# Optimization experiments

Measured on AMD Instinct MI355X. Metric: run time of the kernel, lower is better.

## Reference

```python
import jax, jax.numpy as jnp
import numpy as np

WS = 7      # window size
SHIFT = 3   # shift size
H = 56
W = 56
NH = 16     # num heads


def _layernorm(x, g, b):
    m = x.mean(-1, keepdims=True)
    v = x.var(-1, keepdims=True)
    return (x - m) / jnp.sqrt(v + 1e-5) * g + b


def setup_inputs() -> dict:
    key = jax.random.key(0)
    ks = jax.random.split(key, 8)
    B, C = 16, 512
    DH = 4 * C
    s = 0.02
    x = jax.random.normal(ks[0], (B, H * W, C), jnp.float32)

    # relative position index (matches torch buffer construction)
    coords = np.stack(np.meshgrid(np.arange(WS), np.arange(WS), indexing='ij')).reshape(2, -1)
    rel = (coords[:, :, None] - coords[:, None, :]).transpose(1, 2, 0).copy()
    rel[..., 0] += WS - 1
    rel[..., 1] += WS - 1
    rel[..., 0] *= 2 * WS - 1
    rpi = jnp.asarray(rel.sum(-1), jnp.int32)  # (49, 49)

    # shifted-window additive attention mask (nW, N, N)
    img = np.zeros((H, W))
    cnt = 0
    for hs in (slice(0, -WS), slice(-WS, -SHIFT), slice(-SHIFT, None)):
        for wsl in (slice(0, -WS), slice(-WS, -SHIFT), slice(-SHIFT, None)):
            img[hs, wsl] = cnt
            cnt += 1
    mw = img.reshape(H // WS, WS, W // WS, WS).transpose(0, 2, 1, 3).reshape(-1, WS * WS)
    diff = mw[:, None, :] - mw[:, :, None]  # == mw.unsqueeze(1) - mw.unsqueeze(2)
    attn_mask = jnp.asarray(np.where(diff != 0, -100.0, 0.0), jnp.float32)

    return {
        'x': x,
        'rpi': rpi,
        'attn_mask': attn_mask,
        'norm1_g': jnp.ones((C,), jnp.float32),
        'norm1_b': jnp.zeros((C,), jnp.float32),
        'qkv_w': jax.random.normal(ks[1], (3 * C, C), jnp.float32) * s,
        'qkv_b': jnp.zeros((3 * C,), jnp.float32),
        'proj_w': jax.random.normal(ks[2], (C, C), jnp.float32) * s,
        'proj_b': jnp.zeros((C,), jnp.float32),
        'rpb_table': jax.random.normal(ks[3], ((2 * WS - 1) ** 2, NH), jnp.float32) * s,
        'norm2_g': jnp.ones((C,), jnp.float32),
        'norm2_b': jnp.zeros((C,), jnp.float32),
        'mlp_w1': jax.random.normal(ks[4], (DH, C), jnp.float32) * s,
        'mlp_b1': jnp.zeros((DH,), jnp.float32),
        'mlp_w2': jax.random.normal(ks[5], (C, DH), jnp.float32) * s,
        'mlp_b2': jnp.zeros((C,), jnp.float32),
    }


def reference(x, rpi, attn_mask, norm1_g, norm1_b, qkv_w, qkv_b, proj_w, proj_b,
              rpb_table, norm2_g, norm2_b, mlp_w1, mlp_b1, mlp_w2, mlp_b2):
    B, L, C = x.shape
    N = WS * WS
    nW = (H // WS) * (W // WS)
    hd = C // NH

    # --- attention branch ---
    h = _layernorm(x, norm1_g, norm1_b).reshape(B, H, W, C)
    h = jnp.roll(h, (-SHIFT, -SHIFT), axis=(1, 2))
    # window partition -> (B*nW, N, C)
    xw = h.reshape(B, H // WS, WS, W // WS, WS, C).transpose(0, 1, 3, 2, 4, 5).reshape(B * nW, N, C)

    qkv = (xw @ qkv_w.T + qkv_b).reshape(B * nW, N, 3, NH, hd).transpose(2, 0, 3, 1, 4)
    q, k, v = qkv[0], qkv[1], qkv[2]  # (B*nW, NH, N, hd)
    attn = jnp.einsum('bhnd,bhmd->bhnm', q * (hd ** -0.5), k)
    rpb = rpb_table[rpi].transpose(2, 0, 1)  # (NH, N, N)
    attn = attn + rpb[None]
    attn = attn.reshape(B, nW, NH, N, N) + attn_mask[None, :, None]
    attn = jax.nn.softmax(attn.reshape(B * nW, NH, N, N), axis=-1)
    o = jnp.einsum('bhnm,bhmd->bhnd', attn, v).transpose(0, 2, 1, 3).reshape(B * nW, N, C)
    o = o @ proj_w.T + proj_b
    # window reverse + unshift
    o = o.reshape(B, H // WS, W // WS, WS, WS, C).transpose(0, 1, 3, 2, 4, 5).reshape(B, H, W, C)
    o = jnp.roll(o, (SHIFT, SHIFT), axis=(1, 2)).reshape(B, L, C)

    x = x + o
    # --- MLP branch ---
    h2 = _layernorm(x, norm2_g, norm2_b)
    m = jax.nn.gelu(h2 @ mlp_w1.T + mlp_b1, approximate=False)
    return x + (m @ mlp_w2.T + mlp_b2)
```

## Files before the change

kernel.cpp:

```cpp
#include <hip/hip_runtime.h>
#include <hip/hip_bf16.h>

typedef __attribute__((ext_vector_type(8))) short bf16x8_t;
typedef __attribute__((ext_vector_type(4))) float f32x4_t;

#define LD8(p) (*(const bf16x8_t*)(p))

__device__ __forceinline__ void gll16(const void* g, void* l) {
  __builtin_amdgcn_global_load_lds((const __attribute__((address_space(1))) void*)g,
                                   (__attribute__((address_space(3))) void*)l, 16, 0, 0);
}

__global__ __launch_bounds__(256) void k_cvt(const float* __restrict__ in,
                                             __hip_bfloat16* __restrict__ out, int n) {
  int i = blockIdx.x * 256 + threadIdx.x;
  if (i < n) out[i] = __float2bfloat16(in[i]);
}

__global__ __launch_bounds__(256) void k_cmb(const int* __restrict__ rpi,
                                             const float* __restrict__ tab,
                                             const float* __restrict__ mask,
                                             float* __restrict__ cmbp) {
  int idx = blockIdx.x * 256 + threadIdx.x;
  int jj = idx & 3, lane = (idx >> 2) & 63, tile = (idx >> 8) & 15;
  int h = (idx >> 12) & 15, w6 = idx >> 16;
  int r = (tile >> 2) * 16 + (lane >> 4) * 4 + jj;
  int c = (tile & 3) * 16 + (lane & 15);
  float v = -1e9f;
  if (r < 49 && c < 49) v = tab[rpi[r * 49 + c] * 16 + h] + mask[w6 * 2401 + r * 49 + c];
  cmbp[idx] = v;
}

template<int PERM>
__global__ __launch_bounds__(256) void k_ln(const float* __restrict__ in,
                                            const float* __restrict__ g,
                                            const float* __restrict__ bta,
                                            __hip_bfloat16* __restrict__ out) {
  int token = blockIdx.x;
  int t = threadIdx.x;
  const float2 v = ((const float2*)(in + (size_t)token * 512))[t];
  float s = v.x + v.y, sq = v.x * v.x + v.y * v.y;
  #pragma unroll
  for (int d = 1; d < 64; d <<= 1) { s += __shfl_xor(s, d); sq += __shfl_xor(sq, d); }
  __shared__ float ps[4], pq[4];
  int w = t >> 6;
  if ((t & 63) == 0) { ps[w] = s; pq[w] = sq; }
  __syncthreads();
  s  = ps[0] + ps[1] + ps[2] + ps[3];
  sq = pq[0] + pq[1] + pq[2] + pq[3];
  float mean = s * (1.f / 512.f);
  float inv = rsqrtf(sq * (1.f / 512.f) - mean * mean + 1e-5f);
  size_t dst;
  if (PERM) {
    int b = token / 3136, p = token - b * 3136;
    int i = p / 56, j = p - i * 56;
    int gi = (i + 53) % 56, gj = (j + 53) % 56;
    dst = ((size_t)(((b * 64) + (gi / 7) * 8 + (gj / 7)) * 49) + (gi % 7) * 7 + (gj % 7)) * 512;
  } else {
    dst = (size_t)token * 512;
  }
  int c = t * 2;
  out[dst + c]     = __float2bfloat16((v.x - mean) * inv * g[c] + bta[c]);
  out[dst + c + 1] = __float2bfloat16((v.y - mean) * inv * g[c + 1] + bta[c + 1]);
}

__global__ __launch_bounds__(256) void k_attn(const __hip_bfloat16* __restrict__ qkv,
                                              const float* __restrict__ cmbp,
                                              __hip_bfloat16* __restrict__ o) {
  __shared__ __align__(16) __hip_bfloat16 vt_all[4 * 32 * 72];
  __shared__ __align__(16) __hip_bfloat16 P_all[4 * 64 * 72];
  const int t = threadIdx.x, l = t & 63, w = t >> 6;
  const int bw = blockIdx.x;
  const int head = blockIdx.y * 4 + w;
  const int rr = l & 15, g = l >> 4;
  __hip_bfloat16* vt = vt_all + w * (32 * 72);
  __hip_bfloat16* P  = P_all  + w * (64 * 72);
  const __hip_bfloat16* base = qkv + (size_t)bw * 49 * 1536 + head * 32;
  const bf16x8_t zero8 = {};

  { int d = l >> 1, sg = (l & 1) * 8;
    *(bf16x8_t*)(vt + d * 72 + 48 + sg) = zero8; }
  __builtin_amdgcn_sched_barrier(0);
  #pragma unroll
  for (int it = 0; it < 4; ++it) {
    int idx = l + it * 64;
    if (idx < 196) {
      int j = idx >> 2, sg = (idx & 3) * 8;
      bf16x8_t vv = *(const bf16x8_t*)(base + 1024 + (size_t)j * 1536 + sg);
      #pragma unroll
      for (int s2 = 0; s2 < 8; ++s2) vt[(sg + s2) * 72 + j] = ((__hip_bfloat16*)&vv)[s2];
    }
  }
  bf16x8_t aq[4], bk[4];
  #pragma unroll
  for (int m = 0; m < 4; ++m) {
    int row = m * 16 + rr;
    aq[m] = (row < 49) ? *(const bf16x8_t*)(base + (size_t)row * 1536 + g * 8) : zero8;
    bk[m] = (row < 49) ? *(const bf16x8_t*)(base + 512 + (size_t)row * 1536 + g * 8) : zero8;
  }
  const float4* cp = (const float4*)(cmbp + (size_t)((bw & 63) * 16 + head) * 4096);
  f32x4_t S[4][4];
  #pragma unroll
  for (int tm = 0; tm < 4; ++tm)
    #pragma unroll
    for (int tn = 0; tn < 4; ++tn) {
      float4 cv = cp[(tm * 4 + tn) * 64 + l];
      f32x4_t c0 = { cv.x, cv.y, cv.z, cv.w };
      S[tm][tn] = __builtin_amdgcn_mfma_f32_16x16x32_bf16(aq[tm], bk[tn], c0, 0, 0, 0);
    }
  float sm[4][4];
  #pragma unroll
  for (int tm = 0; tm < 4; ++tm) {
    #pragma unroll
    for (int jj = 0; jj < 4; ++jj) {
      float v = fmaxf(fmaxf(S[tm][0][jj], S[tm][1][jj]), fmaxf(S[tm][2][jj], S[tm][3][jj]));
      v = fmaxf(v, __shfl_xor(v, 1));
      v = fmaxf(v, __shfl_xor(v, 2));
      v = fmaxf(v, __shfl_xor(v, 4));
      v = fmaxf(v, __shfl_xor(v, 8));
      float s = 0.f;
      #pragma unroll
      for (int tn = 0; tn < 4; ++tn) {
        float e = __expf(S[tm][tn][jj] - v);
        S[tm][tn][jj] = e;
        s += e;
      }
      s += __shfl_xor(s, 1); s += __shfl_xor(s, 2); s += __shfl_xor(s, 4); s += __shfl_xor(s, 8);
      sm[tm][jj] = s;
    }
  }
  #pragma unroll
  for (int tm = 0; tm < 4; ++tm)
    #pragma unroll
    for (int tn = 0; tn < 4; ++tn)
      #pragma unroll
      for (int jj = 0; jj < 4; ++jj)
        P[(tm * 16 + g * 4 + jj) * 72 + tn * 16 + rr] = __float2bfloat16(S[tm][tn][jj]);

  f32x4_t O[4][2] = {};
  #pragma unroll
  for (int ks = 0; ks < 2; ++ks) {
    bf16x8_t pa[4], vb[2];
    #pragma unroll
    for (int tm = 0; tm < 4; ++tm)
      pa[tm] = *(const bf16x8_t*)(P + (tm * 16 + rr) * 72 + ks * 32 + g * 8);
    #pragma unroll
    for (int tn = 0; tn < 2; ++tn)
      vb[tn] = *(const bf16x8_t*)(vt + (tn * 16 + rr) * 72 + ks * 32 + g * 8);
    #pragma unroll
    for (int tm = 0; tm < 4; ++tm)
      #pragma unroll
      for (int tn = 0; tn < 2; ++tn)
        O[tm][tn] = __builtin_amdgcn_mfma_f32_16x16x32_bf16(pa[tm], vb[tn], O[tm][tn], 0, 0, 0);
  }
  #pragma unroll
  for (int tm = 0; tm < 4; ++tm) {
    #pragma unroll
    for (int jj = 0; jj < 4; ++jj) {
      int r = tm * 16 + g * 4 + jj;
      if (r < 49) {
        float rcp = 1.f / sm[tm][jj];
        size_t ob = ((size_t)bw * 49 + r) * 512 + head * 32;
        o[ob + rr]      = __float2bfloat16(O[tm][0][jj] * rcp);
        o[ob + 16 + rr] = __float2bfloat16(O[tm][1][jj] * rcp);
      }
    }
  }
}

template<int EP>
__global__ __launch_bounds__(512, 2) void gemm256(const __hip_bfloat16* __restrict__ A,
                                                  const __hip_bfloat16* __restrict__ Bw,
                                                  int K, int Ncols, int nNB,
                                                  const float* __restrict__ bias,
                                                  __hip_bfloat16* __restrict__ obf,
                                                  const float* __restrict__ resid,
                                                  float* __restrict__ ofp) {
  __shared__ __align__(16) char LDS[131072];
  const int nwg = gridDim.x, orig = blockIdx.x;
  const int q8 = nwg >> 3, r8 = nwg & 7;
  const int xcd = orig & 7, lin = orig >> 3;
  const int wgid = (xcd < r8 ? xcd * (q8 + 1) : r8 * (q8 + 1) + (xcd - r8) * q8) + lin;
  const int bx = wgid / nNB, by = wgid - bx * nNB;
  const int m0 = bx * 256, n0 = by * 256;
  const int t = threadIdx.x, l = t & 63, w = t >> 6;
  const int wr = w >> 2, wc = w & 3;
  const int rr = l & 15, kq = l >> 4;
  const int swzo = (kq * 16) ^ ((rr & 8) << 2);

  int rs0, cs0, rs1, cs1;
  { int d = t * 16;  rs0 = (d >> 10) * 16 + ((d >> 6) & 15);
    cs0 = ((d & 63) ^ (((d >> 9) & 1) << 5)) >> 1; }
  { int d = 8192 + t * 16; int dd = d & 8191;
    rs1 = (dd >> 10) * 16 + ((dd >> 6) & 15);
    cs1 = 32 + (((d & 63) ^ (((d >> 9) & 1) << 5)) >> 1); }
  const __hip_bfloat16* gA = A + (size_t)m0 * K;
  const __hip_bfloat16* gB = Bw + (size_t)n0 * K;

  auto stageA = [&](int T, int h) {
    char* dst = LDS + (T & 1) * 32768 + h * 16384 + t * 16;
    const size_t kb = (size_t)T * 64;
    gll16(gA + (size_t)(h * 128 + rs0) * K + kb + cs0, dst);
    gll16(gA + (size_t)(h * 128 + rs1) * K + kb + cs1, dst + 8192);
  };
  auto stageB = [&](int T, int h) {
    char* dst = LDS + 65536 + (T & 1) * 32768 + h * 16384 + t * 16;
    const size_t kb = (size_t)T * 64;
    gll16(gB + (size_t)(h * 128 + rs0) * K + kb + cs0, dst);
    gll16(gB + (size_t)(h * 128 + rs1) * K + kb + cs1, dst + 8192);
  };

  auto ldA = [&](bf16x8_t (&a)[4][2], int buf, int mq) {
    const char* b = LDS + buf * 32768 + wr * 16384;
    #pragma unroll
    for (int m = 0; m < 4; ++m)
      #pragma unroll
      for (int ks = 0; ks < 2; ++ks)
        a[m][ks] = *(const bf16x8_t*)(b + ks * 8192 + (mq * 4 + m) * 1024 + rr * 64 + swzo);
  };
  auto ldB = [&](bf16x8_t (&bv)[2][2], int buf, int nq) {
    const char* b = LDS + 65536 + buf * 32768 + (wc >> 1) * 16384;
    #pragma unroll
    for (int n = 0; n < 2; ++n)
      #pragma unroll
      for (int ks = 0; ks < 2; ++ks)
        bv[n][ks] = *(const bf16x8_t*)(b + ks * 8192 + ((wc & 1) * 4 + nq * 2 + n) * 1024 + rr * 64 + swzo);
  };

  f32x4_t acc[8][4] = {};
  auto mma = [&](bf16x8_t (&a)[4][2], bf16x8_t (&bv)[2][2], int mq, int nq) {
    __builtin_amdgcn_s_setprio(1);
    #pragma unroll
    for (int m = 0; m < 4; ++m)
      #pragma unroll
      for (int n = 0; n < 2; ++n)
        #pragma unroll
        for (int ks = 0; ks < 2; ++ks)
          acc[mq * 4 + m][nq * 2 + n] =
            __builtin_amdgcn_mfma_f32_16x16x32_bf16(a[m][ks], bv[n][ks], acc[mq * 4 + m][nq * 2 + n], 0, 0, 0);
    __builtin_amdgcn_s_setprio(0);
  };

  const int NT = K >> 6;
  stageA(0, 0); stageB(0, 0); stageA(0, 1); stageB(0, 1);
  if (1 < NT) { stageA(1, 0); stageB(1, 0); }
  if (1 < NT) asm volatile("s_waitcnt vmcnt(4)" ::: "memory");
  else        asm volatile("s_waitcnt vmcnt(0)" ::: "memory");
  __builtin_amdgcn_s_barrier();

  for (int kt = 0; kt < NT; ++kt) {
    const int cur = kt & 1;
    bf16x8_t Alo[4][2], Ahi[4][2], B0[2][2], B1[2][2];
    ldA(Alo, cur, 0); ldB(B0, cur, 0);
    if (kt + 1 < NT) stageA(kt + 1, 1);
    asm volatile("s_waitcnt lgkmcnt(0)" ::: "memory");
    __builtin_amdgcn_sched_barrier(0);
    mma(Alo, B0, 0, 0);
    ldA(Ahi, cur, 1);
    if (kt + 1 < NT) stageB(kt + 1, 1);
    asm volatile("s_waitcnt lgkmcnt(0)" ::: "memory");
    __builtin_amdgcn_sched_barrier(0);
    mma(Ahi, B0, 1, 0);
    __builtin_amdgcn_s_barrier();
    ldB(B1, cur, 1);
    if (kt + 2 < NT) stageA(kt + 2, 0);
    asm volatile("s_waitcnt lgkmcnt(0)" ::: "memory");
    __builtin_amdgcn_sched_barrier(0);
    mma(Ahi, B1, 1, 1);
    if (kt + 2 < NT) stageB(kt + 2, 0);
    mma(Alo, B1, 0, 1);
    if (kt + 1 < NT) {
      if (kt + 2 < NT) asm volatile("s_waitcnt vmcnt(4)" ::: "memory");
      else             asm volatile("s_waitcnt vmcnt(0)" ::: "memory");
    }
    __builtin_amdgcn_s_barrier();
  }

  #pragma unroll
  for (int m = 0; m < 8; ++m) {
    #pragma unroll
    for (int n = 0; n < 4; ++n) {
      const int gcol = n0 + wc * 64 + n * 16 + rr;
      #pragma unroll
      for (int j = 0; j < 4; ++j) {
        const int grow = m0 + wr * 128 + m * 16 + kq * 4 + j;
        float v = acc[m][n][j] + bias[gcol];
        if (EP == 0) {
          if (gcol < 512) v *= 0.17677669529663687f;
          obf[(size_t)grow * Ncols + gcol] = __float2bfloat16(v);
        } else if (EP == 1) {
          int bw = grow / 49, nn = grow - bw * 49;
          int b = bw >> 6, wi = bw & 63;
          int hh = (wi >> 3) * 7 + nn / 7 + 3;  if (hh >= 56) hh -= 56;
          int ww2 = (wi & 7) * 7 + (nn % 7) + 3; if (ww2 >= 56) ww2 -= 56;
          size_t tok = (size_t)b * 3136 + hh * 56 + ww2;
          ofp[tok * 512 + gcol] = resid[tok * 512 + gcol] + v;
        } else if (EP == 2) {
          float u = 0.5f * v * (1.f + erff(v * 0.70710678118f));
          obf[(size_t)grow * Ncols + gcol] = __float2bfloat16(u);
        } else {
          ofp[(size_t)grow * 512 + gcol] += v;
        }
      }
    }
  }
}

extern "C" void kernel_launch(void* const* d_in, const int* in_sizes, int n_in,
                              void* d_out, int out_size, void* d_ws, size_t ws_size,
                              hipStream_t stream) {
  const float* x      = (const float*)d_in[0];
  const int*   rpi    = (const int*)  d_in[1];
  const float* amask  = (const float*)d_in[2];
  const float* n1g    = (const float*)d_in[3];
  const float* n1b    = (const float*)d_in[4];
  const float* qkv_w  = (const float*)d_in[5];
  const float* qkv_b  = (const float*)d_in[6];
  const float* proj_w = (const float*)d_in[7];
  const float* proj_b = (const float*)d_in[8];
  const float* rpb_t  = (const float*)d_in[9];
  const float* n2g    = (const float*)d_in[10];
  const float* n2b    = (const float*)d_in[11];
  const float* w1     = (const float*)d_in[12];
  const float* b1     = (const float*)d_in[13];
  const float* w2     = (const float*)d_in[14];
  const float* b2     = (const float*)d_in[15];
  float* out = (float*)d_out;

  char* ws = (char*)d_ws;
  const size_t M = 50176;
  const size_t szA = M * 2048 * 2;
  const size_t szB = M * 1536 * 2;
  const size_t offB = szA;
  const size_t offW = offB + szB;
  __hip_bfloat16* bufA = (__hip_bfloat16*)(ws);
  __hip_bfloat16* bufB = (__hip_bfloat16*)(ws + offB);
  __hip_bfloat16* wqkv  = (__hip_bfloat16*)(ws + offW);
  __hip_bfloat16* wproj = wqkv + 786432;
  __hip_bfloat16* wm1   = wproj + 262144;
  __hip_bfloat16* wm2   = wm1 + 1048576;
  float* cmbp = (float*)(ws + szA - (size_t)4194304 * 4);

  k_cvt<<<3072, 256, 0, stream>>>(qkv_w, wqkv, 786432);
  k_cvt<<<1024, 256, 0, stream>>>(proj_w, wproj, 262144);
  k_cvt<<<4096, 256, 0, stream>>>(w1, wm1, 1048576);
  k_cvt<<<4096, 256, 0, stream>>>(w2, wm2, 1048576);
  k_cmb<<<16384, 256, 0, stream>>>(rpi, rpb_t, amask, cmbp);

  k_ln<1><<<50176, 256, 0, stream>>>(x, n1g, n1b, bufA);
  gemm256<0><<<196 * 6, 512, 0, stream>>>(bufA, wqkv, 512, 1536, 6, qkv_b, bufB, nullptr, nullptr);
  k_attn<<<dim3(1024, 4), 256, 0, stream>>>(bufB, cmbp, bufA);
  gemm256<1><<<196 * 2, 512, 0, stream>>>(bufA, wproj, 512, 512, 2, proj_b, nullptr, x, out);
  k_ln<0><<<50176, 256, 0, stream>>>(out, n2g, n2b, bufB);
  gemm256<2><<<196 * 8, 512, 0, stream>>>(bufB, wm1, 512, 2048, 8, b1, bufA, nullptr, nullptr);
  gemm256<3><<<196 * 2, 512, 0, stream>>>(bufA, wm2, 2048, 512, 2, b2, nullptr, nullptr, out);
}
```

Measured before the change: 808.0 us.

## Vectorize layernorm and weight conversion, drop explicit LDS waits in GEMM

New measurement: 761.9 us. 1.06x faster.

```diff
diff --git a/kernel.cpp b/kernel.cpp
--- a/kernel.cpp
+++ b/kernel.cpp
@@ -3,18 +3,29 @@
 
 typedef __attribute__((ext_vector_type(8))) short bf16x8_t;
 typedef __attribute__((ext_vector_type(4))) float f32x4_t;
-
-#define LD8(p) (*(const bf16x8_t*)(p))
 
 __device__ __forceinline__ void gll16(const void* g, void* l) {
   __builtin_amdgcn_global_load_lds((const __attribute__((address_space(1))) void*)g,
                                    (__attribute__((address_space(3))) void*)l, 16, 0, 0);
 }
 
-__global__ __launch_bounds__(256) void k_cvt(const float* __restrict__ in,
-                                             __hip_bfloat16* __restrict__ out, int n) {
-  int i = blockIdx.x * 256 + threadIdx.x;
-  if (i < n) out[i] = __float2bfloat16(in[i]);
+__global__ __launch_bounds__(256) void k_cvt4(const float* __restrict__ s0, const float* __restrict__ s1,
+                                              const float* __restrict__ s2, const float* __restrict__ s3,
+                                              __hip_bfloat16* __restrict__ out) {
+  int i4 = blockIdx.x * 256 + threadIdx.x;
+  int i = i4 * 4;
+  const float* src;
+  int off;
+  if (i < 786432)       { src = s0; off = i; }
+  else if (i < 1048576) { src = s1; off = i - 786432; }
+  else if (i < 2097152) { src = s2; off = i - 1048576; }
+  else                  { src = s3; off = i - 2097152; }
+  float4 v = *(const float4*)(src + off);
+  union { __hip_bfloat16 h[4]; ushort2 u2[2]; } pk;
+  pk.h[0] = __float2bfloat16(v.x); pk.h[1] = __float2bfloat16(v.y);
+  pk.h[2] = __float2bfloat16(v.z); pk.h[3] = __float2bfloat16(v.w);
+  *(ushort2*)(out + i) = pk.u2[0];
+  *(ushort2*)(out + i + 2) = pk.u2[1];
 }
 
 __global__ __launch_bounds__(256) void k_cmb(const int* __restrict__ rpi,
@@ -36,32 +47,38 @@
                                             const float* __restrict__ g,
                                             const float* __restrict__ bta,
                                             __hip_bfloat16* __restrict__ out) {
-  int token = blockIdx.x;
-  int t = threadIdx.x;
-  const float2 v = ((const float2*)(in + (size_t)token * 512))[t];
-  float s = v.x + v.y, sq = v.x * v.x + v.y * v.y;
+  const int w = threadIdx.x >> 6, l = threadIdx.x & 63;
+  const int token = blockIdx.x * 4 + w;
+  const float4* p = (const float4*)(in + (size_t)token * 512);
+  float4 v0 = p[l], v1 = p[l + 64];
+  float s  = v0.x + v0.y + v0.z + v0.w + v1.x + v1.y + v1.z + v1.w;
+  float sq = v0.x*v0.x + v0.y*v0.y + v0.z*v0.z + v0.w*v0.w
+           + v1.x*v1.x + v1.y*v1.y + v1.z*v1.z + v1.w*v1.w;
   #pragma unroll
   for (int d = 1; d < 64; d <<= 1) { s += __shfl_xor(s, d); sq += __shfl_xor(sq, d); }
-  __shared__ float ps[4], pq[4];
-  int w = t >> 6;
-  if ((t & 63) == 0) { ps[w] = s; pq[w] = sq; }
-  __syncthreads();
-  s  = ps[0] + ps[1] + ps[2] + ps[3];
-  sq = pq[0] + pq[1] + pq[2] + pq[3];
   float mean = s * (1.f / 512.f);
   float inv = rsqrtf(sq * (1.f / 512.f) - mean * mean + 1e-5f);
   size_t dst;
   if (PERM) {
-    int b = token / 3136, p = token - b * 3136;
-    int i = p / 56, j = p - i * 56;
+    int b = token / 3136, pp = token - b * 3136;
+    int i = pp / 56, j = pp - i * 56;
     int gi = (i + 53) % 56, gj = (j + 53) % 56;
     dst = ((size_t)(((b * 64) + (gi / 7) * 8 + (gj / 7)) * 49) + (gi % 7) * 7 + (gj % 7)) * 512;
   } else {
     dst = (size_t)token * 512;
   }
-  int c = t * 2;
-  out[dst + c]     = __float2bfloat16((v.x - mean) * inv * g[c] + bta[c]);
-  out[dst + c + 1] = __float2bfloat16((v.y - mean) * inv * g[c + 1] + bta[c + 1]);
+  int c0 = l * 4, c1 = 256 + l * 4;
+  union { __hip_bfloat16 h[4]; ushort4 u4; } a, b4;
+  a.h[0] = __float2bfloat16((v0.x - mean) * inv * g[c0]     + bta[c0]);
+  a.h[1] = __float2bfloat16((v0.y - mean) * inv * g[c0 + 1] + bta[c0 + 1]);
+  a.h[2] = __float2bfloat16((v0.z - mean) * inv * g[c0 + 2] + bta[c0 + 2]);
+  a.h[3] = __float2bfloat16((v0.w - mean) * inv * g[c0 + 3] + bta[c0 + 3]);
+  b4.h[0] = __float2bfloat16((v1.x - mean) * inv * g[c1]     + bta[c1]);
+  b4.h[1] = __float2bfloat16((v1.y - mean) * inv * g[c1 + 1] + bta[c1 + 1]);
+  b4.h[2] = __float2bfloat16((v1.z - mean) * inv * g[c1 + 2] + bta[c1 + 2]);
+  b4.h[3] = __float2bfloat16((v1.w - mean) * inv * g[c1 + 3] + bta[c1 + 3]);
+  *(ushort4*)(out + dst + c0) = a.u4;
+  *(ushort4*)(out + dst + c1) = b4.u4;
 }
 
 __global__ __launch_bounds__(256) void k_attn(const __hip_bfloat16* __restrict__ qkv,
@@ -253,19 +270,13 @@
     bf16x8_t Alo[4][2], Ahi[4][2], B0[2][2], B1[2][2];
     ldA(Alo, cur, 0); ldB(B0, cur, 0);
     if (kt + 1 < NT) stageA(kt + 1, 1);
-    asm volatile("s_waitcnt lgkmcnt(0)" ::: "memory");
-    __builtin_amdgcn_sched_barrier(0);
     mma(Alo, B0, 0, 0);
     ldA(Ahi, cur, 1);
     if (kt + 1 < NT) stageB(kt + 1, 1);
-    asm volatile("s_waitcnt lgkmcnt(0)" ::: "memory");
-    __builtin_amdgcn_sched_barrier(0);
     mma(Ahi, B0, 1, 0);
     __builtin_amdgcn_s_barrier();
     ldB(B1, cur, 1);
     if (kt + 2 < NT) stageA(kt + 2, 0);
-    asm volatile("s_waitcnt lgkmcnt(0)" ::: "memory");
-    __builtin_amdgcn_sched_barrier(0);
     mma(Ahi, B1, 1, 1);
     if (kt + 2 < NT) stageB(kt + 2, 0);
     mma(Alo, B1, 0, 1);
@@ -336,22 +347,19 @@
   __hip_bfloat16* bufA = (__hip_bfloat16*)(ws);
   __hip_bfloat16* bufB = (__hip_bfloat16*)(ws + offB);
   __hip_bfloat16* wqkv  = (__hip_bfloat16*)(ws + offW);
+  float* cmbp = (float*)(ws + szA - (size_t)4194304 * 4);
   __hip_bfloat16* wproj = wqkv + 786432;
   __hip_bfloat16* wm1   = wproj + 262144;
   __hip_bfloat16* wm2   = wm1 + 1048576;
-  float* cmbp = (float*)(ws + szA - (size_t)4194304 * 4);
-
-  k_cvt<<<3072, 256, 0, stream>>>(qkv_w, wqkv, 786432);
-  k_cvt<<<1024, 256, 0, stream>>>(proj_w, wproj, 262144);
-  k_cvt<<<4096, 256, 0, stream>>>(w1, wm1, 1048576);
-  k_cvt<<<4096, 256, 0, stream>>>(w2, wm2, 1048576);
+
+  k_cvt4<<<3072, 256, 0, stream>>>(qkv_w, proj_w, w1, w2, wqkv);
   k_cmb<<<16384, 256, 0, stream>>>(rpi, rpb_t, amask, cmbp);
 
-  k_ln<1><<<50176, 256, 0, stream>>>(x, n1g, n1b, bufA);
+  k_ln<1><<<12544, 256, 0, stream>>>(x, n1g, n1b, bufA);
   gemm256<0><<<196 * 6, 512, 0, stream>>>(bufA, wqkv, 512, 1536, 6, qkv_b, bufB, nullptr, nullptr);
   k_attn<<<dim3(1024, 4), 256, 0, stream>>>(bufB, cmbp, bufA);
   gemm256<1><<<196 * 2, 512, 0, stream>>>(bufA, wproj, 512, 512, 2, proj_b, nullptr, x, out);
-  k_ln<0><<<50176, 256, 0, stream>>>(out, n2g, n2b, bufB);
+  k_ln<0><<<12544, 256, 0, stream>>>(out, n2g, n2b, bufB);
   gemm256<2><<<196 * 8, 512, 0, stream>>>(bufB, wm1, 512, 2048, 8, b1, bufA, nullptr, nullptr);
   gemm256<3><<<196 * 2, 512, 0, stream>>>(bufA, wm2, 2048, 512, 2, b2, nullptr, nullptr, out);
 }
```
